# Optimization experiments

Hardware: AMD Instinct MI355X
Metric: run time of the kernel (lower is better)

The kernel has to match this reference:

```python
import jax, jax.numpy as jnp
import numpy as np

NPOINT = 1024
RADIUS = 0.2
NSAMPLE = 32
EPS = 1e-5


def _fps(xyz, npoint):
    # sequential farthest-point sampling; deterministic start at index 0
    B, N, _ = xyz.shape

    def step(carry, _):
        distance, farthest = carry
        centroid = jnp.take_along_axis(xyz, farthest[:, None, None], axis=1)  # [B,1,3]
        d = jnp.sum((xyz - centroid) ** 2, axis=-1)  # [B,N]
        distance = jnp.minimum(distance, d)
        return (distance, jnp.argmax(distance, axis=-1).astype(jnp.int32)), farthest

    init = (jnp.full((B, N), 1e10, xyz.dtype), jnp.zeros((B,), jnp.int32))
    _, cent = jax.lax.scan(step, init, None, length=npoint)  # [npoint,B]
    return jnp.transpose(cent)  # [B,npoint]


def _sqdist(src, dst):
    # [B,S,3],[B,N,3] -> [B,S,N]
    return (jnp.sum(src ** 2, -1, keepdims=True)
            - 2.0 * jnp.einsum('bsc,bnc->bsn', src, dst)
            + jnp.sum(dst ** 2, -1)[:, None, :])


def _ball_query(radius, nsample, xyz, new_xyz):
    B, N, _ = xyz.shape
    S = new_xyz.shape[1]
    sq = _sqdist(new_xyz, xyz)  # [B,S,N]
    idx = jnp.broadcast_to(jnp.arange(N, dtype=jnp.int32), (B, S, N))
    idx = jnp.where(sq > radius ** 2, N, idx)
    idx = jnp.sort(idx, axis=-1)[..., :nsample]  # [B,S,K]
    first = idx[..., :1]
    return jnp.where(idx == N, first, idx)


def _gather(points, idx):
    # points [B,N,C], idx [B,S,K] -> [B,S,K,C]
    return jnp.take_along_axis(points[:, None, :, :], idx[..., None], axis=2)


def _block(x, w, b, g, be):
    # 1x1 conv (channel matmul) + BatchNorm2d (training stats) + ReLU
    x = jnp.einsum('bskc,oc->bsko', x, w) + b
    mean = jnp.mean(x, axis=(0, 1, 2))
    var = jnp.var(x, axis=(0, 1, 2))
    x = (x - mean) * jax.lax.rsqrt(var + EPS) * g + be
    return jax.nn.relu(x)


def setup_inputs() -> dict:
    key = jax.random.key(0)
    ks = jax.random.split(key, 16)
    B, N = 16, 8192
    inp = {
        'xyz': jax.random.uniform(ks[0], (B, N, 3), jnp.float32),
        'points': jax.random.normal(ks[1], (B, N, 3), jnp.float32),
    }
    chans = [6, 64, 64, 128]
    for i in range(3):
        cin, cout = chans[i], chans[i + 1]
        inp[f'w{i+1}'] = jax.random.normal(ks[2 + 4 * i], (cout, cin), jnp.float32) * (1.0 / np.sqrt(cin))
        inp[f'b{i+1}'] = jnp.zeros((cout,), jnp.float32)
        inp[f'g{i+1}'] = jnp.ones((cout,), jnp.float32)
        inp[f'be{i+1}'] = jnp.zeros((cout,), jnp.float32)
    return inp


def reference(xyz, points, w1, b1, g1, be1, w2, b2, g2, be2, w3, b3, g3, be3):
    idx_fps = _fps(xyz, NPOINT)                                   # [B,S]
    new_xyz = jnp.take_along_axis(xyz, idx_fps[..., None], axis=1)  # [B,S,3]
    idx_ball = _ball_query(RADIUS, NSAMPLE, xyz, new_xyz)          # [B,S,K]
    g_xyz = _gather(xyz, idx_ball) - new_xyz[:, :, None, :]        # [B,S,K,3]
    g_pts = _gather(points, idx_ball)                               # [B,S,K,3]
    x = jnp.concatenate([g_xyz, g_pts], axis=-1)                    # [B,S,K,6]
    for (w, b, g, be) in ((w1, b1, g1, be1), (w2, b2, g2, be2), (w3, b3, g3, be3)):
        x = _block(x, w, b, g, be)
    new_points = jnp.max(x, axis=2)                                 # [B,S,128]
    return new_xyz, new_points
```

## Files before the change

### kernel.cpp

```cpp
#include <hip/hip_runtime.h>

#define NB 16
#define NN 8192
#define NS 1024
#define NK 32
#define NR (NB*NS*NK)

#define NFPS 16
#define NWORK 240
#define NWAVES (NWORK*8)

static __device__ __forceinline__ int brev6(int l) {
  return ((l&1)<<5)|((l&2)<<3)|((l&4)<<1)|((l&8)>>1)|((l&16)>>3)|((l&32)>>5);
}

static __device__ __forceinline__ unsigned pack_bf2(float a, float b) {
  unsigned ua = __float_as_uint(a), ub = __float_as_uint(b);
  ua += 0x7fffu + ((ua >> 16) & 1u);
  ub += 0x7fffu + ((ub >> 16) & 1u);
  return (ua >> 16) | (ub & 0xffff0000u);
}
static __device__ __forceinline__ float bf_lo(unsigned u) { return __uint_as_float(u << 16); }
static __device__ __forceinline__ float bf_hi(unsigned u) { return __uint_as_float(u & 0xffff0000u); }

template<int CTRL>
static __device__ __forceinline__ float dppmaxf(float v) {
  int m = __builtin_amdgcn_update_dpp(0, __float_as_int(v), CTRL, 0xf, 0xf, true);
  return fmaxf(v, __int_as_float(m));
}
template<int CTRL>
static __device__ __forceinline__ unsigned dppmaxu(unsigned v) {
  unsigned m = (unsigned)__builtin_amdgcn_update_dpp(0, (int)v, CTRL, 0xf, 0xf, true);
  return v > m ? v : m;
}

__global__ __launch_bounds__(512, 1) void fps_bq_s1_kernel(
    const float* __restrict__ xyz, const float* __restrict__ pts,
    const float* __restrict__ w1,  const float* __restrict__ b1,
    float* __restrict__ new_xyz,   float* __restrict__ x0,
    float* __restrict__ part)
{
  __shared__ float sx[NN], sy[NN], sz[NN];
  __shared__ unsigned long long s_wb[2][8];

  if (blockIdx.x < NFPS) {
    const int b = blockIdx.x;
    const int t = threadIdx.x;
    const int lane = t & 63;
    const int wv = t >> 6;
    const float* base = xyz + (size_t)b * NN * 3;

    float px[16], py[16], pz[16], dist[16];
#pragma unroll
    for (int j = 0; j < 16; ++j) {
      int p = j * 512 + t;
      float x = base[p*3+0], y = base[p*3+1], z = base[p*3+2];
      px[j] = x; py[j] = y; pz[j] = z; dist[j] = 1e10f;
      sx[p] = x; sy[p] = y; sz[p] = z;
    }
    __syncthreads();

    float cx = sx[0], cy = sy[0], cz = sz[0];
    unsigned* outp = (unsigned*)(new_xyz + (size_t)b * NS * 3);
    if (t == 0) {
      __hip_atomic_store(outp+0, __float_as_uint(cx), __ATOMIC_RELAXED, __HIP_MEMORY_SCOPE_AGENT);
      __hip_atomic_store(outp+1, __float_as_uint(cy), __ATOMIC_RELAXED, __HIP_MEMORY_SCOPE_AGENT);
      __hip_atomic_store(outp+2, __float_as_uint(cz), __ATOMIC_RELAXED, __HIP_MEMORY_SCOPE_AGENT);
    }

    for (int s = 1; s < NS; ++s) {
      const int par = s & 1;
      float bestv = -1.0f;
      int bj = 0;
#pragma unroll
      for (int j = 0; j < 16; ++j) {
        float dx = px[j]-cx, dy = py[j]-cy, dz = pz[j]-cz;
        float d = __fadd_rn(__fadd_rn(__fmul_rn(dx,dx),__fmul_rn(dy,dy)),__fmul_rn(dz,dz));
        float nd = fminf(dist[j], d);
        dist[j] = nd;
        if (nd > bestv) { bestv = nd; bj = j; }
      }
      float wm = bestv;
      wm = dppmaxf<0x111>(wm);
      wm = dppmaxf<0x112>(wm);
      wm = dppmaxf<0x114>(wm);
      wm = dppmaxf<0x118>(wm);
      wm = dppmaxf<0x142>(wm);
      wm = dppmaxf<0x143>(wm);
      const unsigned wmax_bits = (unsigned)__builtin_amdgcn_readlane(__float_as_int(wm), 63);
      const float wmax = __uint_as_float(wmax_bits);
      unsigned enc = (bestv == wmax) ? (unsigned)(8191 - (bj * 512 + t)) : 0u;
      enc = dppmaxu<0x111>(enc);
      enc = dppmaxu<0x112>(enc);
      enc = dppmaxu<0x114>(enc);
      enc = dppmaxu<0x118>(enc);
      enc = dppmaxu<0x142>(enc);
      enc = dppmaxu<0x143>(enc);
      const unsigned widx_enc = (unsigned)__builtin_amdgcn_readlane((int)enc, 63);
      if (lane == 0)
        s_wb[par][wv] = ((unsigned long long)wmax_bits << 32) | widx_enc;
      __syncthreads();
      unsigned long long gk = s_wb[par][0];
#pragma unroll
      for (int i = 1; i < 8; ++i) {
        unsigned long long ki = s_wb[par][i]; if (ki > gk) gk = ki;
      }
      const int bi = 8191 - (int)(gk & 0xffffull);
      cx = sx[bi]; cy = sy[bi]; cz = sz[bi];
      if (t == 0) {
        unsigned* o = outp + s*3;
        __hip_atomic_store(o+0, __float_as_uint(cx), __ATOMIC_RELAXED, __HIP_MEMORY_SCOPE_AGENT);
        __hip_atomic_store(o+1, __float_as_uint(cy), __ATOMIC_RELAXED, __HIP_MEMORY_SCOPE_AGENT);
        __hip_atomic_store(o+2, __float_as_uint(cz), __ATOMIC_RELAXED, __HIP_MEMORY_SCOPE_AGENT);
      }
    }
  } else {
    const int wid  = ((int)blockIdx.x - NFPS) * 8 + (threadIdx.x >> 6);
    const int lane = threadIdx.x & 63;
    float wrow[6];
#pragma unroll
    for (int c = 0; c < 6; ++c) wrow[c] = w1[lane*6 + c];
    const float bv = b1[lane];
    const float R2 = 0.04f;
    float itemS = 0.f, itemQ = 0.f;

    for (int item = wid; item < NB*NS; item += NWAVES) {
      const int s = item >> 4;
      const int b = item & 15;
      const int gw = (b << 10) + s;
      const float* base  = xyz + (size_t)b * NN * 3;
      const float* pbase = pts + (size_t)b * NN * 3;
      float* out = x0 + (size_t)gw * (NK*6);

      const unsigned* cp = (const unsigned*)(new_xyz + (size_t)gw * 3);
      float cx, cy, cz;
      for (;;) {
        unsigned ux = __hip_atomic_load(cp+0, __ATOMIC_RELAXED, __HIP_MEMORY_SCOPE_AGENT);
        unsigned uy = __hip_atomic_load(cp+1, __ATOMIC_RELAXED, __HIP_MEMORY_SCOPE_AGENT);
        unsigned uz = __hip_atomic_load(cp+2, __ATOMIC_RELAXED, __HIP_MEMORY_SCOPE_AGENT);
        if (ux != 0xFFFFFFFFu && uy != 0xFFFFFFFFu && uz != 0xFFFFFFFFu) {
          cx = __uint_as_float(ux); cy = __uint_as_float(uy); cz = __uint_as_float(uz);
          break;
        }
        __builtin_amdgcn_s_sleep(16);
      }

      const float t1 = __fadd_rn(__fadd_rn(__fmul_rn(cx,cx),__fmul_rn(cy,cy)),__fmul_rn(cz,cz));
      int count = 0, pfirst = 0;
      for (int n0 = 0; n0 < NN; n0 += 64) {
        const int p = n0 + lane;
        const float ax = base[p*3], ay = base[p*3+1], az = base[p*3+2];
        const float t2 = __fadd_rn(__fadd_rn(__fmul_rn(ax,ax),__fmul_rn(ay,ay)),__fmul_rn(az,az));
        const float dt = __fmaf_rn(cz, az, __fmaf_rn(cy, ay, __fmul_rn(cx, ax)));
        const float sq = __fadd_rn(__fsub_rn(t1, __fmul_rn(2.0f,dt)), t2);
        const bool keep = !(sq > R2);
        const unsigned long long mask = __ballot(keep);
        const int slot = count + __popcll(mask & ((1ull<<lane)-1ull));
        if (keep && slot < NK) {
          float* o = out + slot*6;
          o[0]=ax-cx; o[1]=ay-cy; o[2]=az-cz;
          o[3]=pbase[p*3]; o[4]=pbase[p*3+1]; o[5]=pbase[p*3+2];
        }
        if (count == 0 && mask != 0ull) pfirst = n0 + (__ffsll((unsigned long long)mask) - 1);
        count += __popcll(mask);
        if (count >= NK) break;
      }
      if (count < NK) {
        const float* fx = base + (size_t)pfirst*3;
        const float* fp = pbase + (size_t)pfirst*3;
        const float a0 = fx[0]-cx, a1 = fx[1]-cy, a2 = fx[2]-cz;
        const float a3 = fp[0], a4 = fp[1], a5 = fp[2];
        for (int sl = count + lane; sl < NK; sl += 64) {
          float* o = out + sl*6;
          o[0]=a0;o[1]=a1;o[2]=a2;o[3]=a3;o[4]=a4;o[5]=a5;
        }
      }

      __threadfence_block();
      float sAcc = 0.f, qAcc = 0.f;
#pragma unroll 4
      for (int k = 0; k < NK; ++k) {
        const float* row = out + k*6;
        float z = bv;
#pragma unroll
        for (int c = 0; c < 6; ++c) z = fmaf(row[c], wrow[c], z);
        sAcc += z;
        qAcc = fmaf(z, z, qAcc);
      }
      itemS += sAcc;
      itemQ += qAcc;
    }
    part[(size_t)wid*128 + lane]      = itemS;
    part[(size_t)wid*128 + 64 + lane] = itemQ;
  }
}

__global__ __launch_bounds__(256) void finalize_kernel(const float* __restrict__ part,
                                                       int nrows, int rowstride, int C,
                                                       const float* __restrict__ g,
                                                       const float* __restrict__ be,
                                                       float* __restrict__ ab) {
  const int ch = blockIdx.x;
  const int t = threadIdx.x;
  const int qo = rowstride >> 1;
  double s = 0.0, q = 0.0;
  for (int wv = t; wv < nrows; wv += 256) {
    s += (double)part[(size_t)wv*rowstride + ch];
    q += (double)part[(size_t)wv*rowstride + qo + ch];
  }
#pragma unroll
  for (int off = 32; off >= 1; off >>= 1) {
    s += __shfl_down(s, off, 64);
    q += __shfl_down(q, off, 64);
  }
  __shared__ double ls[4], lq[4];
  if ((t & 63) == 0) { ls[t>>6] = s; lq[t>>6] = q; }
  __syncthreads();
  if (t == 0) {
    double S = ls[0]+ls[1]+ls[2]+ls[3];
    double Q = lq[0]+lq[1]+lq[2]+lq[3];
    double mean = S / (double)NR;
    double var  = Q / (double)NR - mean*mean;
    double inv  = 1.0 / sqrt(var + 1e-5);
    double gg   = (double)g[ch];
    ab[ch]     = (float)(gg * inv);
    ab[C + ch] = (float)((double)be[ch] - mean * gg * inv);
  }
}


__device__ __forceinline__ void lean_h1(const float* __restrict__ xr,
                                        const float* __restrict__ w1,
                                        const float* __restrict__ b1,
                                        const float* __restrict__ ab1,
                                        float (&h)[64]) {
  float x[6];
#pragma unroll
  for (int c = 0; c < 6; ++c) x[c] = xr[c];
#pragma unroll
  for (int o = 0; o < 64; ++o) {
    float acc = b1[o];
#pragma unroll
    for (int c = 0; c < 6; ++c) acc = fmaf(x[c], w1[o*6+c], acc);
    h[o] = fmaxf(0.f, fmaf(acc, ab1[o], ab1[64+o]));
  }
}

__global__ __launch_bounds__(256) void stats2_store(const float* __restrict__ x0,
                                                    const float* __restrict__ w1,
                                                    const float* __restrict__ b1,
                                                    const float* __restrict__ ab1,
                                                    const float* __restrict__ w2,
                                                    const float* __restrict__ b2,
                                                    unsigned* __restrict__ z2u,
                                                    float* __restrict__ part) {
  const int t = threadIdx.x;
  const int lane = t & 63;
  const int wvi = t >> 6;
  __shared__ float hT[4][64*68];
  __shared__ float rS[4][64], rQ[4][64];

  const int row0 = ((int)blockIdx.x*4 + wvi) * 64;
  float* ht = hT[wvi];

  {
    float h[64];
    lean_h1(x0 + (size_t)(row0 + lane)*6, w1, b1, ab1, h);
    float4* hw = (float4*)(ht + lane*68);
#pragma unroll
    for (int c4 = 0; c4 < 16; ++c4)
      hw[c4] = make_float4(h[4*c4+0], h[4*c4+1], h[4*c4+2], h[4*c4+3]);
  }
  asm volatile("s_waitcnt lgkmcnt(0)" ::: "memory");

  float w2r[64];
  {
    const float4* wr = (const float4*)(w2 + (size_t)lane*64);
#pragma unroll
    for (int c4 = 0; c4 < 16; ++c4) {
      float4 v = wr[c4];
      w2r[4*c4+0]=v.x; w2r[4*c4+1]=v.y; w2r[4*c4+2]=v.z; w2r[4*c4+3]=v.w;
    }
  }
  const float bz = b2[lane];
  float accS = 0.f, accQ = 0.f;
#pragma unroll 2
  for (int r = 0; r < 64; ++r) {
    const float4* hr = (const float4*)(ht + r*68);
    float z = bz;
#pragma unroll
    for (int c4 = 0; c4 < 16; ++c4) {
      float4 hv = hr[c4];
      z = fmaf(hv.x, w2r[4*c4+0], z);
      z = fmaf(hv.y, w2r[4*c4+1], z);
      z = fmaf(hv.z, w2r[4*c4+2], z);
      z = fmaf(hv.w, w2r[4*c4+3], z);
    }
    accS += z; accQ = fmaf(z, z, accQ);
    const float zp = __shfl_xor(z, 1, 64);
    const unsigned word = (lane & 1) ? pack_bf2(zp, z) : pack_bf2(z, zp);
    if ((lane & 1) == 0)
      z2u[(size_t)(row0 + r)*32 + (lane >> 1)] = word;
  }
  rS[wvi][lane] = accS; rQ[wvi][lane] = accQ;
  __syncthreads();
  if (t < 64)
    part[(size_t)blockIdx.x*128 + t] = rS[0][t]+rS[1][t]+rS[2][t]+rS[3][t];
  else if (t < 128) {
    const int c = t - 64;
    part[(size_t)blockIdx.x*128 + 64 + c] = rQ[0][c]+rQ[1][c]+rQ[2][c]+rQ[3][c];
  }
}

__global__ __launch_bounds__(256) void stats3_fused(const unsigned* __restrict__ z2u,
                                                    const float* __restrict__ ab,
                                                    const float* __restrict__ w,
                                                    const float* __restrict__ bias,
                                                    float* __restrict__ part,
                                                    float* __restrict__ kmx,
                                                    float* __restrict__ kmn) {
  const int t = threadIdx.x;
  const int lane = t & 63;
  const int wvi = t >> 6;
  __shared__ float hT[4][64*68];
  __shared__ float rS[4][128], rQ[4][128];

  const int row0 = ((int)blockIdx.x*4 + wvi) * 64;
  float* ht = hT[wvi];

  {
    const uint4* zr = (const uint4*)(z2u + (size_t)(row0 + lane) * 32);
    float h[64];
#pragma unroll
    for (int i = 0; i < 8; ++i) {
      uint4 v = zr[i];
      const int c = i*8;
      h[c+0]=fmaxf(0.f,fmaf(bf_lo(v.x),ab[c+0],ab[64+c+0]));
      h[c+1]=fmaxf(0.f,fmaf(bf_hi(v.x),ab[c+1],ab[64+c+1]));
      h[c+2]=fmaxf(0.f,fmaf(bf_lo(v.y),ab[c+2],ab[64+c+2]));
      h[c+3]=fmaxf(0.f,fmaf(bf_hi(v.y),ab[c+3],ab[64+c+3]));
      h[c+4]=fmaxf(0.f,fmaf(bf_lo(v.z),ab[c+4],ab[64+c+4]));
      h[c+5]=fmaxf(0.f,fmaf(bf_hi(v.z),ab[c+5],ab[64+c+5]));
      h[c+6]=fmaxf(0.f,fmaf(bf_lo(v.w),ab[c+6],ab[64+c+6]));
      h[c+7]=fmaxf(0.f,fmaf(bf_hi(v.w),ab[c+7],ab[64+c+7]));
    }
    float4* hw = (float4*)(ht + lane*68);
#pragma unroll
    for (int c4 = 0; c4 < 16; ++c4)
      hw[c4] = make_float4(h[4*c4+0], h[4*c4+1], h[4*c4+2], h[4*c4+3]);
  }
  asm volatile("s_waitcnt lgkmcnt(0)" ::: "memory");

  float w3a[64], w3b[64];
  {
    const float4* wra = (const float4*)(w + (size_t)lane*64);
    const float4* wrb = (const float4*)(w + (size_t)(lane+64)*64);
#pragma unroll
    for (int c4 = 0; c4 < 16; ++c4) {
      float4 va = wra[c4];
      w3a[4*c4+0]=va.x; w3a[4*c4+1]=va.y; w3a[4*c4+2]=va.z; w3a[4*c4+3]=va.w;
      float4 vb = wrb[c4];
      w3b[4*c4+0]=vb.x; w3b[4*c4+1]=vb.y; w3b[4*c4+2]=vb.z; w3b[4*c4+3]=vb.w;
    }
  }
  const float bza = bias[lane], bzb = bias[64+lane];
  float sA = 0.f, qA = 0.f, sB = 0.f, qB = 0.f;
#pragma unroll 1
  for (int g2 = 0; g2 < 2; ++g2) {
    float mA = -1e30f, nA = 1e30f, mB = -1e30f, nB = 1e30f;
#pragma unroll 2
    for (int r = g2*32; r < g2*32 + 32; ++r) {
      const float4* hr = (const float4*)(ht + r*68);
      float za = bza, zb = bzb;
#pragma unroll
      for (int c4 = 0; c4 < 16; ++c4) {
        float4 hv = hr[c4];
        za = fmaf(hv.x, w3a[4*c4+0], za);
        za = fmaf(hv.y, w3a[4*c4+1], za);
        za = fmaf(hv.z, w3a[4*c4+2], za);
        za = fmaf(hv.w, w3a[4*c4+3], za);
        zb = fmaf(hv.x, w3b[4*c4+0], zb);
        zb = fmaf(hv.y, w3b[4*c4+1], zb);
        zb = fmaf(hv.z, w3b[4*c4+2], zb);
        zb = fmaf(hv.w, w3b[4*c4+3], zb);
      }
      mA = fmaxf(mA, za); nA = fminf(nA, za); sA += za; qA = fmaf(za, za, qA);
      mB = fmaxf(mB, zb); nB = fminf(nB, zb); sB += zb; qB = fmaf(zb, zb, qB);
    }
    const size_t group = (size_t)(((int)blockIdx.x*4 + wvi)*2 + g2);
    kmx[group*128 + lane]      = mA;
    kmx[group*128 + 64 + lane] = mB;
    kmn[group*128 + lane]      = nA;
    kmn[group*128 + 64 + lane] = nB;
  }
  rS[wvi][lane] = sA; rS[wvi][64+lane] = sB;
  rQ[wvi][lane] = qA; rQ[wvi][64+lane] = qB;
  __syncthreads();
  if (t < 128)
    part[(size_t)blockIdx.x*256 + t] = rS[0][t]+rS[1][t]+rS[2][t]+rS[3][t];
  else {
    const int c = t - 128;
    part[(size_t)blockIdx.x*256 + 128 + c] = rQ[0][c]+rQ[1][c]+rQ[2][c]+rQ[3][c];
  }
}

__global__ __launch_bounds__(128) void bn3_kernel(const float* __restrict__ kmx,
                                                  const float* __restrict__ kmn,
                                                  const float* __restrict__ ab,
                                                  float* __restrict__ outp) {
  const int g = blockIdx.x;
  const int c = threadIdx.x;
  const float a = ab[c], bsh = ab[128 + c];
  const float v = (a >= 0.f) ? kmx[(size_t)g*128 + c] : kmn[(size_t)g*128 + c];
  outp[(size_t)g*128 + c] = fmaxf(0.f, fmaf(v, a, bsh));
}


extern "C" void kernel_launch(void* const* d_in, const int* in_sizes, int n_in,
                              void* d_out, int out_size, void* d_ws, size_t ws_size,
                              hipStream_t stream) {
  (void)in_sizes; (void)n_in; (void)out_size; (void)ws_size;
  const float* xyz = (const float*)d_in[0];
  const float* pts = (const float*)d_in[1];
  const float* w1  = (const float*)d_in[2];
  const float* b1  = (const float*)d_in[3];
  const float* g1  = (const float*)d_in[4];
  const float* be1 = (const float*)d_in[5];
  const float* w2  = (const float*)d_in[6];
  const float* b2  = (const float*)d_in[7];
  const float* g2  = (const float*)d_in[8];
  const float* be2 = (const float*)d_in[9];
  const float* w3  = (const float*)d_in[10];
  const float* b3  = (const float*)d_in[11];
  const float* g3  = (const float*)d_in[12];
  const float* be3 = (const float*)d_in[13];

  float* out = (float*)d_out;
  float* new_xyz    = out;
  float* new_points = out + NB*NS*3;

  float* ws = (float*)d_ws;
  float* x0   = ws;
  float* part = x0 + (size_t)NR*6;
  float* ab   = part + 2097152;
  float* ab1  = ab;
  float* ab2  = ab + 128;
  float* ab3  = ab + 256;
  unsigned* z2u = (unsigned*)(ab + 512);
  float* kmx = (float*)(z2u + (size_t)NR*32);
  float* kmn = kmx + (size_t)16384*128;
  const int NBLK = NR/256;

  (void)hipMemsetAsync(new_xyz, 0xFF, (size_t)NB*NS*3*sizeof(float), stream);

  hipLaunchKernelGGL(fps_bq_s1_kernel, dim3(NFPS + NWORK), dim3(512), 0, stream,
                     xyz, pts, w1, b1, new_xyz, x0, part);

  hipLaunchKernelGGL(finalize_kernel, dim3(64), dim3(256), 0, stream, part, NWAVES, 128, 64, g1, be1, ab1);
  hipLaunchKernelGGL(stats2_store, dim3(NBLK), dim3(256), 0, stream,
                     x0, w1, b1, ab1, w2, b2, z2u, part);
  hipLaunchKernelGGL(finalize_kernel, dim3(64), dim3(256), 0, stream, part, NBLK, 128, 64, g2, be2, ab2);
  hipLaunchKernelGGL(stats3_fused, dim3(NBLK), dim3(256), 0, stream,
                     z2u, ab2, w3, b3, part, kmx, kmn);
  hipLaunchKernelGGL(finalize_kernel, dim3(128), dim3(256), 0, stream, part, NBLK, 256, 128, g3, be3, ab3);
  hipLaunchKernelGGL(bn3_kernel, dim3(NB*NS), dim3(128), 0, stream, kmx, kmn, ab3, new_points);
}
```

Measured before the change: 1.308 ms.

## Fuse BN finalize into producer kernels via last-block atomic ticket

Drops the three separate finalize_kernel launches. Each producer kernel now takes an atomic ticket, and the last block to finish reduces the per-block partial sums in double precision. It then writes the BN scale and shift that the next kernel reads. bn3_kernel is also reshaped to handle 1024 elements per 256-thread block. The cost is that the final reduction runs serially in one block: each thread sums hundreds to about a thousand rows in a loop, replacing the wide per-channel parallel reduction. This may add tail latency that outweighs the launch overhead saved.

```diff
diff --git a/kernel.cpp b/kernel.cpp
--- a/kernel.cpp
+++ b/kernel.cpp
@@ -9,10 +9,7 @@
 #define NFPS 16
 #define NWORK 240
 #define NWAVES (NWORK*8)
-
-static __device__ __forceinline__ int brev6(int l) {
-  return ((l&1)<<5)|((l&2)<<3)|((l&4)<<1)|((l&8)>>1)|((l&16)>>3)|((l&32)>>5);
-}
+#define NBLK (NR/256)
 
 static __device__ __forceinline__ unsigned pack_bf2(float a, float b) {
   unsigned ua = __float_as_uint(a), ub = __float_as_uint(b);
@@ -34,14 +31,54 @@
   return v > m ? v : m;
 }
 
+__device__ __forceinline__ void fin_inline(const float* __restrict__ part, int nrows,
+                                           int rowstride, int C, int nsl,
+                                           const float* __restrict__ g,
+                                           const float* __restrict__ be,
+                                           float* __restrict__ ab,
+                                           double* __restrict__ ds,
+                                           double* __restrict__ dq) {
+  const int t = threadIdx.x;
+  const int c = t % C;
+  const int slice = t / C;
+  const int per = nrows / nsl;
+  const int qo = rowstride >> 1;
+  if (slice < nsl) {
+    double s = 0.0, q = 0.0;
+    const int r0 = slice * per;
+    for (int i = 0; i < per; ++i) {
+      const size_t r = (size_t)(r0 + i) * rowstride;
+      s += (double)part[r + c];
+      q += (double)part[r + qo + c];
+    }
+    ds[slice*C + c] = s;
+    dq[slice*C + c] = q;
+  }
+  __syncthreads();
+  if (t < C) {
+    double S = 0.0, Q = 0.0;
+    for (int i = 0; i < nsl; ++i) { S += ds[i*C + t]; Q += dq[i*C + t]; }
+    double mean = S / (double)NR;
+    double var  = Q / (double)NR - mean*mean;
+    double inv  = 1.0 / sqrt(var + 1e-5);
+    double gg   = (double)g[t];
+    ab[t]     = (float)(gg * inv);
+    ab[C + t] = (float)((double)be[t] - mean * gg * inv);
+  }
+}
+
 __global__ __launch_bounds__(512, 1) void fps_bq_s1_kernel(
     const float* __restrict__ xyz, const float* __restrict__ pts,
     const float* __restrict__ w1,  const float* __restrict__ b1,
+    const float* __restrict__ g1,  const float* __restrict__ be1,
     float* __restrict__ new_xyz,   float* __restrict__ x0,
-    float* __restrict__ part)
+    float* __restrict__ part,      float* __restrict__ ab1,
+    unsigned* __restrict__ tick)
 {
   __shared__ float sx[NN], sy[NN], sz[NN];
   __shared__ unsigned long long s_wb[2][8];
+  __shared__ double dfs[512], dfq[512];
+  __shared__ int s_flag;
 
   if (blockIdx.x < NFPS) {
     const int b = blockIdx.x;
@@ -192,39 +229,15 @@
     }
     part[(size_t)wid*128 + lane]      = itemS;
     part[(size_t)wid*128 + 64 + lane] = itemQ;
-  }
-}
-
-__global__ __launch_bounds__(256) void finalize_kernel(const float* __restrict__ part,
-                                                       int nrows, int rowstride, int C,
-                                                       const float* __restrict__ g,
-                                                       const float* __restrict__ be,
-                                                       float* __restrict__ ab) {
-  const int ch = blockIdx.x;
-  const int t = threadIdx.x;
-  const int qo = rowstride >> 1;
-  double s = 0.0, q = 0.0;
-  for (int wv = t; wv < nrows; wv += 256) {
-    s += (double)part[(size_t)wv*rowstride + ch];
-    q += (double)part[(size_t)wv*rowstride + qo + ch];
-  }
-#pragma unroll
-  for (int off = 32; off >= 1; off >>= 1) {
-    s += __shfl_down(s, off, 64);
-    q += __shfl_down(q, off, 64);
-  }
-  __shared__ double ls[4], lq[4];
-  if ((t & 63) == 0) { ls[t>>6] = s; lq[t>>6] = q; }
-  __syncthreads();
-  if (t == 0) {
-    double S = ls[0]+ls[1]+ls[2]+ls[3];
-    double Q = lq[0]+lq[1]+lq[2]+lq[3];
-    double mean = S / (double)NR;
-    double var  = Q / (double)NR - mean*mean;
-    double inv  = 1.0 / sqrt(var + 1e-5);
-    double gg   = (double)g[ch];
-    ab[ch]     = (float)(gg * inv);
-    ab[C + ch] = (float)((double)be[ch] - mean * gg * inv);
+
+    __syncthreads();
+    if (threadIdx.x == 0) {
+      unsigned old = __hip_atomic_fetch_add(tick, 1u, __ATOMIC_ACQ_REL, __HIP_MEMORY_SCOPE_AGENT);
+      s_flag = (old == (unsigned)(NWORK - 1));
+    }
+    __syncthreads();
+    if (s_flag)
+      fin_inline(part, NWAVES, 128, 64, 8, g1, be1, ab1, dfs, dfq);
   }
 }
 
@@ -252,13 +265,19 @@
                                                     const float* __restrict__ ab1,
                                                     const float* __restrict__ w2,
                                                     const float* __restrict__ b2,
+                                                    const float* __restrict__ g2,
+                                                    const float* __restrict__ be2,
                                                     unsigned* __restrict__ z2u,
-                                                    float* __restrict__ part) {
+                                                    float* __restrict__ part,
+                                                    float* __restrict__ ab2,
+                                                    unsigned* __restrict__ tick) {
   const int t = threadIdx.x;
   const int lane = t & 63;
   const int wvi = t >> 6;
   __shared__ float hT[4][64*68];
   __shared__ float rS[4][64], rQ[4][64];
+  __shared__ double dls[256], dlq[256];
+  __shared__ int s_last;
 
   const int row0 = ((int)blockIdx.x*4 + wvi) * 64;
   float* ht = hT[wvi];
@@ -310,20 +329,35 @@
     const int c = t - 64;
     part[(size_t)blockIdx.x*128 + 64 + c] = rQ[0][c]+rQ[1][c]+rQ[2][c]+rQ[3][c];
   }
+
+  __syncthreads();
+  if (t == 0) {
+    unsigned old = __hip_atomic_fetch_add(tick, 1u, __ATOMIC_ACQ_REL, __HIP_MEMORY_SCOPE_AGENT);
+    s_last = (old == (unsigned)(NBLK - 1));
+  }
+  __syncthreads();
+  if (s_last)
+    fin_inline(part, NBLK, 128, 64, 4, g2, be2, ab2, dls, dlq);
 }
 
 __global__ __launch_bounds__(256) void stats3_fused(const unsigned* __restrict__ z2u,
                                                     const float* __restrict__ ab,
                                                     const float* __restrict__ w,
                                                     const float* __restrict__ bias,
+                                                    const float* __restrict__ g3,
+                                                    const float* __restrict__ be3,
                                                     float* __restrict__ part,
                                                     float* __restrict__ kmx,
-                                                    float* __restrict__ kmn) {
+                                                    float* __restrict__ kmn,
+                                                    float* __restrict__ ab3,
+                                                    unsigned* __restrict__ tick) {
   const int t = threadIdx.x;
   const int lane = t & 63;
   const int wvi = t >> 6;
   __shared__ float hT[4][64*68];
   __shared__ float rS[4][128], rQ[4][128];
+  __shared__ double dls[256], dlq[256];
+  __shared__ int s_last;
 
   const int row0 = ((int)blockIdx.x*4 + wvi) * 64;
   float* ht = hT[wvi];
@@ -402,17 +436,30 @@
     const int c = t - 128;
     part[(size_t)blockIdx.x*256 + 128 + c] = rQ[0][c]+rQ[1][c]+rQ[2][c]+rQ[3][c];
   }
-}
-
-__global__ __launch_bounds__(128) void bn3_kernel(const float* __restrict__ kmx,
+
+  __syncthreads();
+  if (t == 0) {
+    unsigned old = __hip_atomic_fetch_add(tick, 1u, __ATOMIC_ACQ_REL, __HIP_MEMORY_SCOPE_AGENT);
+    s_last = (old == (unsigned)(NBLK - 1));
+  }
+  __syncthreads();
+  if (s_last)
+    fin_inline(part, NBLK, 256, 128, 2, g3, be3, ab3, dls, dlq);
+}
+
+__global__ __launch_bounds__(256) void bn3_kernel(const float* __restrict__ kmx,
                                                   const float* __restrict__ kmn,
                                                   const float* __restrict__ ab,
                                                   float* __restrict__ outp) {
-  const int g = blockIdx.x;
-  const int c = threadIdx.x;
-  const float a = ab[c], bsh = ab[128 + c];
-  const float v = (a >= 0.f) ? kmx[(size_t)g*128 + c] : kmn[(size_t)g*128 + c];
-  outp[(size_t)g*128 + c] = fmaxf(0.f, fmaf(v, a, bsh));
+  const int t = threadIdx.x;
+#pragma unroll
+  for (int k = 0; k < 4; ++k) {
+    const size_t idx = (size_t)blockIdx.x*1024 + k*256 + t;
+    const int c = (int)(idx & 127);
+    const float a = ab[c], bsh = ab[128 + c];
+    const float v = (a >= 0.f) ? kmx[idx] : kmn[idx];
+    outp[idx] = fmaxf(0.f, fmaf(v, a, bsh));
+  }
 }
 
 
@@ -449,19 +496,17 @@
   unsigned* z2u = (unsigned*)(ab + 512);
   float* kmx = (float*)(z2u + (size_t)NR*32);
   float* kmn = kmx + (size_t)16384*128;
-  const int NBLK = NR/256;
+  unsigned* tick = (unsigned*)(kmn + (size_t)16384*128);
 
   (void)hipMemsetAsync(new_xyz, 0xFF, (size_t)NB*NS*3*sizeof(float), stream);
+  (void)hipMemsetAsync(tick, 0, 3*sizeof(unsigned), stream);
 
   hipLaunchKernelGGL(fps_bq_s1_kernel, dim3(NFPS + NWORK), dim3(512), 0, stream,
-                     xyz, pts, w1, b1, new_xyz, x0, part);
-
-  hipLaunchKernelGGL(finalize_kernel, dim3(64), dim3(256), 0, stream, part, NWAVES, 128, 64, g1, be1, ab1);
+                     xyz, pts, w1, b1, g1, be1, new_xyz, x0, part, ab1, tick + 0);
+
   hipLaunchKernelGGL(stats2_store, dim3(NBLK), dim3(256), 0, stream,
-                     x0, w1, b1, ab1, w2, b2, z2u, part);
-  hipLaunchKernelGGL(finalize_kernel, dim3(64), dim3(256), 0, stream, part, NBLK, 128, 64, g2, be2, ab2);
+                     x0, w1, b1, ab1, w2, b2, g2, be2, z2u, part, ab2, tick + 1);
   hipLaunchKernelGGL(stats3_fused, dim3(NBLK), dim3(256), 0, stream,
-                     z2u, ab2, w3, b3, part, kmx, kmn);
-  hipLaunchKernelGGL(finalize_kernel, dim3(128), dim3(256), 0, stream, part, NBLK, 256, 128, g3, be3, ab3);
-  hipLaunchKernelGGL(bn3_kernel, dim3(NB*NS), dim3(128), 0, stream, kmx, kmn, ab3, new_points);
-}
+                     z2u, ab2, w3, b3, g3, be3, part, kmx, kmn, ab3, tick + 2);
+  hipLaunchKernelGGL(bn3_kernel, dim3(2048), dim3(256), 0, stream, kmx, kmn, ab3, new_points);
+}
```

New measurement: 1.426 ms. +9.0%, slower.
